# Optimization experiments

Hardware: AMD Instinct MI355X
Metric: run time of the kernel (lower is better)

Reference implementation:

```python
import jax, jax.numpy as jnp
import numpy as np

B, T, I, H = 8, 2048, 512, 512


def _lstm(x_tbi, Wih, Whh, bih, bhh):
    # x_tbi: [T, B, I]; torch LSTMCell gate order: input, forget, cell(g), output
    h0 = jnp.zeros((x_tbi.shape[1], Whh.shape[1]), x_tbi.dtype)

    def step(carry, xt):
        h, c = carry
        gates = xt @ Wih.T + bih + h @ Whh.T + bhh  # [B, 4H]
        i, f, g, o = jnp.split(gates, 4, axis=-1)
        c = jax.nn.sigmoid(f) * c + jax.nn.sigmoid(i) * jnp.tanh(g)
        h = jax.nn.sigmoid(o) * jnp.tanh(c)
        return (h, c), h

    (_, _), hs = jax.lax.scan(step, (h0, h0), x_tbi)
    return hs  # [T, B, H]


def setup_inputs() -> dict:
    key = jax.random.key(0)
    ks = jax.random.split(key, 9)
    s = 1.0 / np.sqrt(H)
    mk = lambda k, shp: jax.random.uniform(k, shp, jnp.float32, -s, s)
    return {
        "input": jax.random.normal(ks[0], (B, T, I), jnp.float32),
        "Wih_f": mk(ks[1], (4 * H, I)),
        "Whh_f": mk(ks[2], (4 * H, H)),
        "bih_f": mk(ks[3], (4 * H,)),
        "bhh_f": mk(ks[4], (4 * H,)),
        "Wih_b": mk(ks[5], (4 * H, I)),
        "Whh_b": mk(ks[6], (4 * H, H)),
        "bih_b": mk(ks[7], (4 * H,)),
        "bhh_b": mk(ks[8], (4 * H,)),
    }


def reference(input, Wih_f, Whh_f, bih_f, bhh_f, Wih_b, Whh_b, bih_b, bhh_b):
    x_tbi = jnp.swapaxes(input, 0, 1)  # [T, B, I]
    fwd = _lstm(x_tbi, Wih_f, Whh_f, bih_f, bhh_f)            # [T, B, H]
    bwd = _lstm(x_tbi[::-1], Wih_b, Whh_b, bih_b, bhh_b)      # [T, B, H] on reversed seq
    bwd_rev = bwd[::-1]
    # torch: stack(...).squeeze(1) is a no-op for B>1; cat(-1).unsqueeze(0)
    return jnp.concatenate([fwd, bwd_rev], axis=-1)[None]     # [1, T, B, 2H]
```

## Files before the change

### kernel.cpp

```cpp
#include <hip/hip_runtime.h>
#include <stdint.h>

#define TT 2048
#define BB 8
#define II 512
#define HH 512
#define GG 32
#define HS 16
#define SLOT (BB*HH)
#define SENT32 0x7FC07FC0u

typedef __attribute__((ext_vector_type(8))) short short8;
typedef __attribute__((ext_vector_type(4))) float float4v;
typedef __attribute__((ext_vector_type(2))) float floatx2;
typedef __attribute__((ext_vector_type(4))) unsigned uint4v;

__device__ __forceinline__ unsigned short f2bf(float f) {
  unsigned u = __builtin_bit_cast(unsigned, f);
  u = u + 0x7FFFu + ((u >> 16) & 1u);
  return (unsigned short)(u >> 16);
}

__device__ __forceinline__ float fsigmoid(float x) {
  return __fdividef(1.0f, 1.0f + __expf(-x));
}
__device__ __forceinline__ float ftanh(float x) {
  float e = __expf(-2.0f * fabsf(x));
  float r = __fdividef(1.0f - e, 1.0f + e);
  return x < 0.0f ? -r : r;
}

__global__ void xprep_kernel(const float* __restrict__ x,
                             unsigned short* __restrict__ xbf) {
  int idx = blockIdx.x * 256 + threadIdx.x;
  int k8 = idx & 63;
  int bt = idx >> 6;
  int t  = bt & (TT - 1);
  int b  = bt >> 11;
  const float* src = x + ((size_t)b * TT + t) * II + (size_t)k8 * 8;
  float4v v0 = *(const float4v*)src;
  float4v v1 = *(const float4v*)(src + 4);
  short8 o;
  o[0] = (short)f2bf(v0[0]); o[1] = (short)f2bf(v0[1]);
  o[2] = (short)f2bf(v0[2]); o[3] = (short)f2bf(v0[3]);
  o[4] = (short)f2bf(v1[0]); o[5] = (short)f2bf(v1[1]);
  o[6] = (short)f2bf(v1[2]); o[7] = (short)f2bf(v1[3]);
  *(short8*)(xbf + ((size_t)t * BB + b) * II + (size_t)k8 * 8) = o;
}

__global__ void hinit_kernel(unsigned short* __restrict__ hh) {
  size_t e8   = ((size_t)blockIdx.x * 256 + threadIdx.x) * 8;
  size_t slot = (e8 / SLOT) % (TT + 1);
  short v = (slot == 0) ? (short)0 : (short)0x7FC0;
  short8 o = {v, v, v, v, v, v, v, v};
  *(short8*)(hh + e8) = o;
}

__global__ __launch_bounds__(256, 1) void lstm_kernel(
    const float* __restrict__ Wih_f, const float* __restrict__ Whh_f,
    const float* __restrict__ bih_f, const float* __restrict__ bhh_f,
    const float* __restrict__ Wih_b, const float* __restrict__ Whh_b,
    const float* __restrict__ bih_b, const float* __restrict__ bhh_b,
    const unsigned short* __restrict__ xbf,
    unsigned short* __restrict__ h_hist,
    float* __restrict__ out)
{
  const int dir  = blockIdx.x >> 5;
  const int wg   = blockIdx.x & 31;
  const int tid  = threadIdx.x;
  const int wave = tid >> 6;
  const int lane = tid & 63;
  const int m    = lane & 15;
  const int q    = lane >> 4;
  const bool nv  = (m < BB);

  const float* __restrict__ Wih = dir ? Wih_b : Wih_f;
  const float* __restrict__ Whh = dir ? Whh_b : Whh_f;
  const float* __restrict__ bih = dir ? bih_b : bih_f;
  const float* __restrict__ bhh = dir ? bhh_b : bhh_f;

  const int j0   = wg * HS;
  const int grow = wave * HH + j0 + m;

  short8 a_x[16], a_h[16];
#pragma unroll
  for (int kf = 0; kf < 16; ++kf) {
    const float* p1 = Wih + (size_t)grow * II + kf * 32 + q * 8;
    const float* p2 = Whh + (size_t)grow * HH + kf * 32 + q * 8;
    short8 A, Bv;
#pragma unroll
    for (int j = 0; j < 8; ++j) {
      A[j]  = (short)f2bf(p1[j]);
      Bv[j] = (short)f2bf(p2[j]);
    }
    a_x[kf] = A;
    a_h[kf] = Bv;
  }

  const int ebb = lane >> 3;
  const int ej  = (lane & 7) * 2;
  float c0 = 0.0f, c1 = 0.0f;
  float bi0 = 0.f, bf0 = 0.f, bg0 = 0.f, bo0 = 0.f;
  float bi1 = 0.f, bf1 = 0.f, bg1 = 0.f, bo1 = 0.f;
  if (wave == 0) {
    int ja = j0 + ej, jb = ja + 1;
    bi0 = bih[0 * HH + ja] + bhh[0 * HH + ja];
    bf0 = bih[1 * HH + ja] + bhh[1 * HH + ja];
    bg0 = bih[2 * HH + ja] + bhh[2 * HH + ja];
    bo0 = bih[3 * HH + ja] + bhh[3 * HH + ja];
    bi1 = bih[0 * HH + jb] + bhh[0 * HH + jb];
    bf1 = bih[1 * HH + jb] + bhh[1 * HH + jb];
    bg1 = bih[2 * HH + jb] + bhh[2 * HH + jb];
    bo1 = bih[3 * HH + jb] + bhh[3 * HH + jb];
  }

  __shared__ float lds_g[4][16][17];

  unsigned short* __restrict__ hh = h_hist + (size_t)dir * (TT + 1) * SLOT;
  int bailleft = 2000000;

#pragma unroll 1
  for (int s = 0; s < TT; ++s) {
    const int t = dir ? (TT - 1 - s) : s;

    float4v acc[4];
#pragma unroll
    for (int i = 0; i < 4; ++i) acc[i] = (float4v){0.f, 0.f, 0.f, 0.f};

    {
      const unsigned short* xrow =
          xbf + ((size_t)t * BB + (nv ? m : 0)) * II + q * 8;
      short8 bx[16];
#pragma unroll
      for (int kf = 0; kf < 16; ++kf) {
        short8 v = {0, 0, 0, 0, 0, 0, 0, 0};
        if (nv) v = *(const short8*)(xrow + kf * 32);
        bx[kf] = v;
      }
#pragma unroll
      for (int kf = 0; kf < 16; ++kf)
        acc[kf & 3] = __builtin_amdgcn_mfma_f32_16x16x32_bf16(
            a_x[kf], bx[kf], acc[kf & 3], 0, 0, 0);
    }

    short8 bh[16];
    {
      const unsigned short* hrow =
          hh + (size_t)s * SLOT + (size_t)(nv ? m : 0) * HH + q * 8;
      for (;;) {
#pragma unroll
        for (int kf = 0; kf < 16; ++kf)
          asm volatile("global_load_dwordx4 %0, %1, off sc0 sc1"
                       : "=&v"(bh[kf]) : "v"(hrow + kf * 32) : "memory");
        asm volatile("s_waitcnt vmcnt(0)" ::: "memory");
        unsigned bad = 0u;
#pragma unroll
        for (int kf = 0; kf < 16; ++kf) {
          uint4v u = __builtin_bit_cast(uint4v, bh[kf]);
          bad |= (unsigned)(u[0] == SENT32) | (unsigned)(u[1] == SENT32) |
                 (unsigned)(u[2] == SENT32) | (unsigned)(u[3] == SENT32);
        }
        if (__ballot(bad != 0u) == 0ull) break;
        if (--bailleft < 0) break;
      }
    }
    __builtin_amdgcn_sched_barrier(0);

#pragma unroll
    for (int kf = 0; kf < 16; ++kf)
      acc[kf & 3] = __builtin_amdgcn_mfma_f32_16x16x32_bf16(
          a_h[kf], bh[kf], acc[kf & 3], 0, 0, 0);

#pragma unroll
    for (int r = 0; r < 4; ++r) {
      float g = acc[0][r] + acc[1][r] + acc[2][r] + acc[3][r];
      lds_g[wave][q * 4 + r][m] = g;
    }
    __syncthreads();

    if (wave == 0) {
      float gi0 = lds_g[0][ej + 0][ebb] + bi0;
      float gf0 = lds_g[1][ej + 0][ebb] + bf0;
      float gg0 = lds_g[2][ej + 0][ebb] + bg0;
      float go0 = lds_g[3][ej + 0][ebb] + bo0;
      float gi1 = lds_g[0][ej + 1][ebb] + bi1;
      float gf1 = lds_g[1][ej + 1][ebb] + bf1;
      float gg1 = lds_g[2][ej + 1][ebb] + bg1;
      float go1 = lds_g[3][ej + 1][ebb] + bo1;
      c0 = fsigmoid(gf0) * c0 + fsigmoid(gi0) * ftanh(gg0);
      c1 = fsigmoid(gf1) * c1 + fsigmoid(gi1) * ftanh(gg1);
      float hv0 = fsigmoid(go0) * ftanh(c0);
      float hv1 = fsigmoid(go1) * ftanh(c1);
      unsigned pack = (unsigned)f2bf(hv0) | ((unsigned)f2bf(hv1) << 16);
      unsigned* hp = (unsigned*)(hh + (size_t)(s + 1) * SLOT +
                                 (size_t)ebb * HH + j0 + ej);
      __hip_atomic_store(hp, pack, __ATOMIC_RELAXED, __HIP_MEMORY_SCOPE_AGENT);
      floatx2 o2 = {hv0, hv1};
      __builtin_nontemporal_store(
          o2, (floatx2*)&out[((size_t)t * BB + ebb) * (2 * HH) +
                             (size_t)dir * HH + j0 + ej]);
    }
  }
}

extern "C" void kernel_launch(void* const* d_in, const int* in_sizes, int n_in,
                              void* d_out, int out_size, void* d_ws, size_t ws_size,
                              hipStream_t stream) {
  (void)in_sizes; (void)n_in; (void)out_size; (void)ws_size;
  const float* input = (const float*)d_in[0];
  const float* Wih_f = (const float*)d_in[1];
  const float* Whh_f = (const float*)d_in[2];
  const float* bih_f = (const float*)d_in[3];
  const float* bhh_f = (const float*)d_in[4];
  const float* Wih_b = (const float*)d_in[5];
  const float* Whh_b = (const float*)d_in[6];
  const float* bih_b = (const float*)d_in[7];
  const float* bhh_b = (const float*)d_in[8];

  char* ws = (char*)d_ws;
  unsigned short* xbf    = (unsigned short*)(ws);
  unsigned short* h_hist = (unsigned short*)(ws + 16777216);

  hipLaunchKernelGGL(hinit_kernel, dim3(8196), dim3(256), 0, stream, h_hist);
  hipLaunchKernelGGL(xprep_kernel, dim3(4096), dim3(256), 0, stream, input, xbf);
  hipLaunchKernelGGL(lstm_kernel, dim3(64), dim3(256), 0, stream,
                     Wih_f, Whh_f, bih_f, bhh_f, Wih_b, Whh_b, bih_b, bhh_b,
                     xbf, h_hist, (float*)d_out);
}
```

Before: 6.402 ms.

## Double-buffer h polling loads and issue x loads ahead of spin

Each step now issues the x-row loads and two independent batches of coherent h-row loads together at the start. While one h batch is checked for sentinel values, the other is already in flight, so the polling loop alternates between two buffers instead of doing serial load-wait-check rounds. The x loads no longer use per-lane predication, and the x MFMAs are placed between the load issue and the h wait. This aims to cut inter-workgroup sync latency on the recurrent critical path, at the cost of more VGPRs, extra memory traffic from redundant polling loads, and a buffer copy when the second batch is the one used.

```diff
diff --git a/kernel.cpp b/kernel.cpp
--- a/kernel.cpp
+++ b/kernel.cpp
@@ -55,6 +55,13 @@
   short8 o = {v, v, v, v, v, v, v, v};
   *(short8*)(hh + e8) = o;
 }
+
+#define ISSUE_X(dst, addr)                                              \
+  asm volatile("global_load_dwordx4 %0, %1, off"                        \
+               : "=&v"(dst) : "v"(addr) : "memory")
+#define ISSUE_H(dst, addr)                                              \
+  asm volatile("global_load_dwordx4 %0, %1, off sc0 sc1"                \
+               : "=&v"(dst) : "v"(addr) : "memory")
 
 __global__ __launch_bounds__(256, 1) void lstm_kernel(
     const float* __restrict__ Wih_f, const float* __restrict__ Whh_f,
@@ -123,53 +130,71 @@
   for (int s = 0; s < TT; ++s) {
     const int t = dir ? (TT - 1 - s) : s;
 
+    asm volatile("s_waitcnt vmcnt(0)" ::: "memory");
+
+    const unsigned short* xrow =
+        xbf + ((size_t)t * BB + (nv ? m : 0)) * II + q * 8;
+    const unsigned short* hrow =
+        hh + (size_t)s * SLOT + (size_t)(nv ? m : 0) * HH + q * 8;
+
+    short8 bx[16], bh0[16], bh1[16];
+#pragma unroll
+    for (int kf = 0; kf < 16; ++kf) ISSUE_X(bx[kf], xrow + kf * 32);
+#pragma unroll
+    for (int kf = 0; kf < 16; ++kf) ISSUE_H(bh0[kf], hrow + kf * 32);
+#pragma unroll
+    for (int kf = 0; kf < 16; ++kf) ISSUE_H(bh1[kf], hrow + kf * 32);
+
+    asm volatile("s_waitcnt vmcnt(32)" ::: "memory");
+    __builtin_amdgcn_sched_barrier(0);
     float4v acc[4];
 #pragma unroll
     for (int i = 0; i < 4; ++i) acc[i] = (float4v){0.f, 0.f, 0.f, 0.f};
-
-    {
-      const unsigned short* xrow =
-          xbf + ((size_t)t * BB + (nv ? m : 0)) * II + q * 8;
-      short8 bx[16];
-#pragma unroll
-      for (int kf = 0; kf < 16; ++kf) {
-        short8 v = {0, 0, 0, 0, 0, 0, 0, 0};
-        if (nv) v = *(const short8*)(xrow + kf * 32);
-        bx[kf] = v;
-      }
-#pragma unroll
-      for (int kf = 0; kf < 16; ++kf)
-        acc[kf & 3] = __builtin_amdgcn_mfma_f32_16x16x32_bf16(
-            a_x[kf], bx[kf], acc[kf & 3], 0, 0, 0);
-    }
-
-    short8 bh[16];
-    {
-      const unsigned short* hrow =
-          hh + (size_t)s * SLOT + (size_t)(nv ? m : 0) * HH + q * 8;
-      for (;;) {
-#pragma unroll
-        for (int kf = 0; kf < 16; ++kf)
-          asm volatile("global_load_dwordx4 %0, %1, off sc0 sc1"
-                       : "=&v"(bh[kf]) : "v"(hrow + kf * 32) : "memory");
-        asm volatile("s_waitcnt vmcnt(0)" ::: "memory");
-        unsigned bad = 0u;
-#pragma unroll
-        for (int kf = 0; kf < 16; ++kf) {
-          uint4v u = __builtin_bit_cast(uint4v, bh[kf]);
-          bad |= (unsigned)(u[0] == SENT32) | (unsigned)(u[1] == SENT32) |
-                 (unsigned)(u[2] == SENT32) | (unsigned)(u[3] == SENT32);
-        }
-        if (__ballot(bad != 0u) == 0ull) break;
-        if (--bailleft < 0) break;
-      }
-    }
-    __builtin_amdgcn_sched_barrier(0);
-
 #pragma unroll
     for (int kf = 0; kf < 16; ++kf)
       acc[kf & 3] = __builtin_amdgcn_mfma_f32_16x16x32_bf16(
-          a_h[kf], bh[kf], acc[kf & 3], 0, 0, 0);
+          a_x[kf], bx[kf], acc[kf & 3], 0, 0, 0);
+
+    int use1 = 0;
+    for (;;) {
+      asm volatile("s_waitcnt vmcnt(16)" ::: "memory");
+      __builtin_amdgcn_sched_barrier(0);
+      unsigned bad = 0u;
+#pragma unroll
+      for (int kf = 0; kf < 16; ++kf) {
+        uint4v u = __builtin_bit_cast(uint4v, bh0[kf]);
+        bad |= (unsigned)(u[0] == SENT32) | (unsigned)(u[1] == SENT32) |
+               (unsigned)(u[2] == SENT32) | (unsigned)(u[3] == SENT32);
+      }
+      if (__ballot(bad != 0u) == 0ull) { use1 = 0; break; }
+      if (--bailleft < 0) { use1 = 0; break; }
+#pragma unroll
+      for (int kf = 0; kf < 16; ++kf) ISSUE_H(bh0[kf], hrow + kf * 32);
+
+      asm volatile("s_waitcnt vmcnt(16)" ::: "memory");
+      __builtin_amdgcn_sched_barrier(0);
+      bad = 0u;
+#pragma unroll
+      for (int kf = 0; kf < 16; ++kf) {
+        uint4v u = __builtin_bit_cast(uint4v, bh1[kf]);
+        bad |= (unsigned)(u[0] == SENT32) | (unsigned)(u[1] == SENT32) |
+               (unsigned)(u[2] == SENT32) | (unsigned)(u[3] == SENT32);
+      }
+      if (__ballot(bad != 0u) == 0ull) { use1 = 1; break; }
+      if (--bailleft < 0) { use1 = 1; break; }
+#pragma unroll
+      for (int kf = 0; kf < 16; ++kf) ISSUE_H(bh1[kf], hrow + kf * 32);
+    }
+    if (__builtin_amdgcn_readfirstlane(use1)) {
+#pragma unroll
+      for (int kf = 0; kf < 16; ++kf) bh0[kf] = bh1[kf];
+    }
+    __builtin_amdgcn_sched_barrier(0);
+
+#pragma unroll
+    for (int kf = 0; kf < 16; ++kf)
+      acc[kf & 3] = __builtin_amdgcn_mfma_f32_16x16x32_bf16(
+          a_h[kf], bh0[kf], acc[kf & 3], 0, 0, 0);
 
 #pragma unroll
     for (int r = 0; r < 4; ++r) {
```

New measurement: 9.404 ms. +46.9%, slower.

## Poll hidden state from one wave and broadcast it through LDS

Applied to the files above, without the earlier changes.

Only wave 0 now polls the global h history with coherent loads and issues the x-row and h loads together, so the x-side MFMAs overlap the h-load latency. Wave 0 then writes the validated h tile into shared memory, and the other three waves read it from there after an extra barrier. This is meant to cut redundant coherent global polling traffic and hide load latency on the serial recurrent critical path. In exchange it adds a __syncthreads and an LDS round trip each step, and wave 0 carries more work. Wave 0's x loads no longer mask the lanes with m >= 8, so those lanes read row 0 instead of zeros, which may be harmless only because those MFMA output columns are never used.

```diff
diff --git a/kernel.cpp b/kernel.cpp
--- a/kernel.cpp
+++ b/kernel.cpp
@@ -55,6 +55,13 @@
   short8 o = {v, v, v, v, v, v, v, v};
   *(short8*)(hh + e8) = o;
 }
+
+#define ISSUE_X(dst, addr)                                              \
+  asm volatile("global_load_dwordx4 %0, %1, off"                        \
+               : "=&v"(dst) : "v"(addr) : "memory")
+#define ISSUE_H(dst, addr)                                              \
+  asm volatile("global_load_dwordx4 %0, %1, off sc0 sc1"                \
+               : "=&v"(dst) : "v"(addr) : "memory")
 
 __global__ __launch_bounds__(256, 1) void lstm_kernel(
     const float* __restrict__ Wih_f, const float* __restrict__ Whh_f,
@@ -115,6 +122,7 @@
   }
 
   __shared__ float lds_g[4][16][17];
+  __shared__ short lds_bh[8][520];
 
   unsigned short* __restrict__ hh = h_hist + (size_t)dir * (TT + 1) * SLOT;
   int bailleft = 2000000;
@@ -127,32 +135,28 @@
 #pragma unroll
     for (int i = 0; i < 4; ++i) acc[i] = (float4v){0.f, 0.f, 0.f, 0.f};
 
-    {
-      const unsigned short* xrow =
-          xbf + ((size_t)t * BB + (nv ? m : 0)) * II + q * 8;
+    short8 bh[16];
+    const unsigned short* xrow =
+        xbf + ((size_t)t * BB + (nv ? m : 0)) * II + q * 8;
+
+    if (wave == 0) {
+      const unsigned short* hrow =
+          hh + (size_t)s * SLOT + (size_t)(nv ? m : 0) * HH + q * 8;
       short8 bx[16];
 #pragma unroll
-      for (int kf = 0; kf < 16; ++kf) {
-        short8 v = {0, 0, 0, 0, 0, 0, 0, 0};
-        if (nv) v = *(const short8*)(xrow + kf * 32);
-        bx[kf] = v;
-      }
+      for (int kf = 0; kf < 16; ++kf) ISSUE_X(bx[kf], xrow + kf * 32);
+#pragma unroll
+      for (int kf = 0; kf < 16; ++kf) ISSUE_H(bh[kf], hrow + kf * 32);
+      asm volatile("s_waitcnt vmcnt(16)" ::: "memory");
+      __builtin_amdgcn_sched_barrier(0);
 #pragma unroll
       for (int kf = 0; kf < 16; ++kf)
         acc[kf & 3] = __builtin_amdgcn_mfma_f32_16x16x32_bf16(
             a_x[kf], bx[kf], acc[kf & 3], 0, 0, 0);
-    }
-
-    short8 bh[16];
-    {
-      const unsigned short* hrow =
-          hh + (size_t)s * SLOT + (size_t)(nv ? m : 0) * HH + q * 8;
+
       for (;;) {
-#pragma unroll
-        for (int kf = 0; kf < 16; ++kf)
-          asm volatile("global_load_dwordx4 %0, %1, off sc0 sc1"
-                       : "=&v"(bh[kf]) : "v"(hrow + kf * 32) : "memory");
         asm volatile("s_waitcnt vmcnt(0)" ::: "memory");
+        __builtin_amdgcn_sched_barrier(0);
         unsigned bad = 0u;
 #pragma unroll
         for (int kf = 0; kf < 16; ++kf) {
@@ -162,9 +166,37 @@
         }
         if (__ballot(bad != 0u) == 0ull) break;
         if (--bailleft < 0) break;
+#pragma unroll
+        for (int kf = 0; kf < 16; ++kf) ISSUE_H(bh[kf], hrow + kf * 32);
       }
-    }
-    __builtin_amdgcn_sched_barrier(0);
+      __builtin_amdgcn_sched_barrier(0);
+      if (nv) {
+#pragma unroll
+        for (int kf = 0; kf < 16; ++kf)
+          *(short8*)&lds_bh[m][kf * 32 + q * 8] = bh[kf];
+      }
+    } else {
+      short8 bx[16];
+#pragma unroll
+      for (int kf = 0; kf < 16; ++kf) {
+        short8 v = {0, 0, 0, 0, 0, 0, 0, 0};
+        if (nv) v = *(const short8*)(xrow + kf * 32);
+        bx[kf] = v;
+      }
+#pragma unroll
+      for (int kf = 0; kf < 16; ++kf)
+        acc[kf & 3] = __builtin_amdgcn_mfma_f32_16x16x32_bf16(
+            a_x[kf], bx[kf], acc[kf & 3], 0, 0, 0);
+    }
+
+    __syncthreads();
+
+    if (wave != 0) {
+      const short* bp = &lds_bh[nv ? m : 0][q * 8];
+#pragma unroll
+      for (int kf = 0; kf < 16; ++kf)
+        bh[kf] = *(const short8*)(bp + kf * 32);
+    }
 
 #pragma unroll
     for (int kf = 0; kf < 16; ++kf)
```

Result: slower. 7.221 ms (+12.8%).
